# Optimization experiments

Measured on AMD Instinct MI355X. Metric: run time of the kernel, lower is better.

## Reference

```python
import jax, jax.numpy as jnp
import numpy as np

B, N_PATCH, DIM, HEADS = 64, 196, 768, 12
WIN = (14, 14)
NUM_REL_DIST = (2 * WIN[0] - 1) * (2 * WIN[1] - 1) + 3  # 732


def _build_rel_pos_index():
    ch, cw = np.arange(WIN[0]), np.arange(WIN[1])
    coords = np.stack(np.meshgrid(ch, cw, indexing='ij'))  # (2, Wh, Ww)
    flat = coords.reshape(2, -1)  # (2, Wh*Ww)
    rel = flat[:, :, None] - flat[:, None, :]  # (2, N, N)
    rel = rel.transpose(1, 2, 0).astype(np.int64)  # (N, N, 2)
    rel[:, :, 0] += WIN[0] - 1
    rel[:, :, 1] += WIN[1] - 1
    rel[:, :, 0] *= 2 * WIN[1] - 1
    n = WIN[0] * WIN[1] + 1
    idx = np.zeros((n, n), dtype=np.int64)
    idx[1:, 1:] = rel.sum(-1)
    idx[0, 0:] = NUM_REL_DIST - 3
    idx[0:, 0] = NUM_REL_DIST - 2
    idx[0, 0] = NUM_REL_DIST - 1
    return jnp.asarray(idx)


def setup_inputs() -> dict:
    key = jax.random.key(0)
    ks = jax.random.split(key, 6)
    d = DIM
    return {
        'x': jax.random.normal(ks[0], (B, N_PATCH + 1, d), dtype=jnp.float32),
        'qkv_w': jax.random.normal(ks[1], (3 * d, d), dtype=jnp.float32) * (d ** -0.5),
        'q_bias': jnp.zeros((d,), dtype=jnp.float32),
        'v_bias': jnp.zeros((d,), dtype=jnp.float32),
        'rpb_table': jax.random.normal(ks[2], (NUM_REL_DIST, HEADS), dtype=jnp.float32) * 0.02,
        'proj_w': jax.random.normal(ks[3], (d, d), dtype=jnp.float32) * (d ** -0.5),
        'proj_b': jnp.zeros((d,), dtype=jnp.float32),
        'rel_pos_index': _build_rel_pos_index(),
    }


def reference(x, qkv_w, q_bias, v_bias, rpb_table, proj_w, proj_b, rel_pos_index):
    Bn, N, C = x.shape
    H = HEADS
    hd = C // H
    scale = hd ** -0.5
    bias = jnp.concatenate([q_bias, jnp.zeros_like(v_bias), v_bias])
    qkv = x @ qkv_w.T + bias  # (B, N, 3C)
    qkv = qkv.reshape(Bn, N, 3, H, hd).transpose(2, 0, 3, 1, 4)  # (3, B, H, N, hd)
    q, k, v = qkv[0] * scale, qkv[1], qkv[2]
    attn = jnp.einsum('bhnd,bhmd->bhnm', q, k)  # (B, H, N, N)
    rpb = rpb_table[rel_pos_index.reshape(-1)].reshape(N, N, H).transpose(2, 0, 1)
    attn = jax.nn.softmax(attn + rpb[None], axis=-1)
    out = jnp.einsum('bhnm,bhmd->bhnd', attn, v)  # (B, H, N, hd)
    out = out.transpose(0, 2, 1, 3).reshape(Bn, N, C)
    return out @ proj_w.T + proj_b
```

## Files before the change

### kernel.cpp

```cpp
#include <hip/hip_runtime.h>
#include <hip/hip_bf16.h>

#define HEADS   12
#define HD      64
#define NTOK    197
#define BATCH   64
#define M_TOK   (BATCH*NTOK)
#define DIMC    768
#define NPAIR   (NTOK*NTOK)
#define MPAD    224

typedef __attribute__((ext_vector_type(8))) short bf16x8;
typedef __attribute__((ext_vector_type(4))) short s16x4;
typedef __attribute__((ext_vector_type(4))) float f32x4;

static __device__ __forceinline__ short f2bf(float f) {
    unsigned u = __float_as_uint(f);
    unsigned r = (u + 0x7FFFu + ((u >> 16) & 1u)) >> 16;
    return (short)r;
}
static __device__ __forceinline__ float bf2f(short s) {
    return __uint_as_float(((unsigned)(unsigned short)s) << 16);
}

#define NX (M_TOK * DIMC)
#define NW (3 * DIMC * DIMC)
#define NP (DIMC * DIMC)
__global__ void cvt_kernel(const float* __restrict__ s0, short* __restrict__ d0,
                           const float* __restrict__ s1, short* __restrict__ d1,
                           const float* __restrict__ s2, short* __restrict__ d2) {
    int i = (blockIdx.x * 256 + threadIdx.x) * 4;
    const float* s; short* d;
    if (i < NX)                { s = s0 + i; d = d0 + i; }
    else if (i < NX + NW)      { s = s1 + (i - NX); d = d1 + (i - NX); }
    else if (i < NX + NW + NP) { s = s2 + (i - NX - NW); d = d2 + (i - NX - NW); }
    else return;
    const float4 v = *(const float4*)s;
    s16x4 b; b[0] = f2bf(v.x); b[1] = f2bf(v.y); b[2] = f2bf(v.z); b[3] = f2bf(v.w);
    *(s16x4*)d = b;
}

#define NRPB (HEADS * 13 * 56 * 64)
__global__ void rpbl_kernel(const float* __restrict__ table,
                            const int* __restrict__ idx,
                            short* __restrict__ rpbl) {
    int i = blockIdx.x * 256 + threadIdx.x;
    if (i >= NRPB) return;
    const int lane = i & 63;
    const int q    = (i >> 6) % 56;
    const int rt   = ((i >> 6) / 56) % 13;
    const int h    = (i >> 6) / (56 * 13);
    const int rg = q / 14, mt = q - rg * 14;
    const int g = lane >> 4, c16 = lane & 15;
    const int n = rt * 16 + g * 4 + rg;
    const int m = mt * 16 + c16;
    float v = 0.f;
    if (n < NTOK && m < NTOK) v = table[idx[n * NTOK + m] * HEADS + h];
    rpbl[i] = f2bf(v);
}

#define STAGE(LA, LB, kt)                                                       \
    _Pragma("unroll")                                                           \
    for (int i = 0; i < 4; ++i) {                                               \
        __builtin_amdgcn_global_load_lds(                                       \
            (const __attribute__((address_space(1))) void*)(aptr[i] + (kt) * 64),\
            (__attribute__((address_space(3))) void*)&(LA)[(wv * 4 + i) * 512], \
            16, 0, 0);                                                          \
        __builtin_amdgcn_global_load_lds(                                       \
            (const __attribute__((address_space(1))) void*)(bptr[i] + (kt) * 64),\
            (__attribute__((address_space(3))) void*)&(LB)[(wv * 4 + i) * 512], \
            16, 0, 0);                                                          \
    }

#define COMPUTE(LA, LB)                                                         \
    _Pragma("unroll")                                                           \
    for (int ks = 0; ks < 2; ++ks) {                                            \
        bf16x8 af[4], bfr[4];                                                   \
        const int kk = (((ks * 4 + g) ^ (c16 & 7)) << 3);    \
        _Pragma("unroll")                                                       \
        for (int i = 0; i < 4; ++i)                                             \
            af[i] = *(const bf16x8*)&(LA)[(wr * 64 + i * 16 + c16) * 64 + kk];  \
        _Pragma("unroll")                                                       \
        for (int j = 0; j < 4; ++j)                                             \
            bfr[j] = *(const bf16x8*)&(LB)[(wc * 64 + j * 16 + c16) * 64 + kk]; \
        _Pragma("unroll")                                                       \
        for (int i = 0; i < 4; ++i)                                             \
            _Pragma("unroll")                                                   \
            for (int j = 0; j < 4; ++j)                                         \
                acc[i][j] = __builtin_amdgcn_mfma_f32_16x16x32_bf16(            \
                    af[i], bfr[j], acc[i][j], 0, 0, 0);                         \
    }

__global__ __launch_bounds__(256) void qkv_gemm_kernel(
    const short* __restrict__ xb, const short* __restrict__ wb,
    const float* __restrict__ qb, const float* __restrict__ vb,
    short* __restrict__ q_ws, short* __restrict__ k_ws,
    short* __restrict__ vt_ws) {
    __shared__ __align__(16) short lds_a0[128 * 64];
    __shared__ __align__(16) short lds_a1[128 * 64];
    __shared__ __align__(16) short lds_bb[2 * 128 * 64];
    const int tid  = threadIdx.x;
    const int lane = tid & 63;
    const int wv   = tid >> 6;
    const int wr   = wv >> 1, wc = wv & 1;
    const int flat = blockIdx.x;
    const int xcd  = flat & 7, pos = flat >> 3;
    const int swz  = ((xcd < 6) ? xcd * 223 : 1338 + (xcd - 6) * 222) + pos;
    const int bm   = swz / 18, bn = swz - bm * 18;
    const int g    = lane >> 4, c16 = lane & 15;

    f32x4 acc[4][4] = {};

    const int lrow = lane >> 3;
    const int lcol = ((lane & 7) ^ lrow) * 8;
    const short* aptr[4];
    const short* bptr[4];
    #pragma unroll
    for (int i = 0; i < 4; ++i) {
        const int r  = (wv * 4 + i) * 8 + lrow;
        int gr = bm * 128 + r; if (gr > M_TOK - 1) gr = M_TOK - 1;
        aptr[i] = xb + (size_t)gr * DIMC + lcol;
        bptr[i] = wb + (size_t)(bn * 128 + r) * DIMC + lcol;
    }

    STAGE(lds_a0, lds_bb, 0);
    __syncthreads();
    #pragma unroll
    for (int kp = 0; kp < 6; ++kp) {
        STAGE(lds_a1, (lds_bb + 8192), 2 * kp + 1);
        COMPUTE(lds_a0, lds_bb);
        __syncthreads();
        if (kp < 5) { STAGE(lds_a0, lds_bb, 2 * kp + 2); }
        COMPUTE(lds_a1, (lds_bb + 8192));
        if (kp < 5) __syncthreads();
    }

    __syncthreads();
    short* t = lds_bb;
    if (bn < 12) {
        const int isq = (bn < 6);
        #pragma unroll
        for (int j = 0; j < 4; ++j) {
            const int col = wc * 64 + j * 16 + c16;
            const int r   = isq ? bn * 128 + col : bn * 128 + col - DIMC;
            const float bias = isq ? qb[r] : 0.0f;
            #pragma unroll
            for (int i = 0; i < 4; ++i) {
                const int tok0 = wr * 64 + i * 16 + (g << 2);
                #pragma unroll
                for (int rg = 0; rg < 4; ++rg) {
                    const int tok = tok0 + rg;
                    const int sw  = ((tok >> 2) & 3) << 4;
                    float val = acc[i][j][rg];
                    if (isq) val = (val + bias) * 0.125f;
                    t[tok * 128 + (col ^ sw)] = f2bf(val);
                }
            }
        }
        __syncthreads();
        short* dst = isq ? q_ws : k_ws;
        const int rbase = isq ? bn * 128 : bn * 128 - DIMC;
        for (int tr = 0; tr < 32; ++tr) {
            const int tok = wv * 32 + tr;
            const int tt  = bm * 128 + tok;
            if (tt >= M_TOK) continue;
            const int bb = tt / NTOK, nn = tt - bb * NTOK;
            const int sw = ((tok >> 2) & 3) << 4;
            #pragma unroll
            for (int half = 0; half < 2; ++half) {
                const int col = half * 64 + lane;
                const int h   = (rbase + half * 64) >> 6;
                dst[(((size_t)bb * HEADS + h) * NTOK + nn) * HD + lane] =
                    t[tok * 128 + (col ^ sw)];
            }
        }
    } else {
        #pragma unroll
        for (int i = 0; i < 4; ++i) {
            const int lt0 = wr * 64 + i * 16 + (g << 2);
            #pragma unroll
            for (int j = 0; j < 4; ++j) {
                const int col  = wc * 64 + j * 16 + c16;
                const int sw   = (col & 7) << 3;
                const float bias = vb[(bn - 12) * 128 + col];
                #pragma unroll
                for (int rg = 0; rg < 4; ++rg)
                    t[col * 128 + ((lt0 + rg) ^ sw)] = f2bf(acc[i][j][rg] + bias);
            }
        }
        __syncthreads();
        for (int cc = 0; cc < 32; ++cc) {
            const int col = cc * 4 + wv;
            const int sw  = (col & 7) << 3;
            const int r   = bn * 128 + col - 1536;
            const int h   = r >> 6, d = r & 63;
            #pragma unroll
            for (int half = 0; half < 2; ++half) {
                const int lt = lane + half * 64;
                const int tt = bm * 128 + lt;
                if (tt < M_TOK) {
                    const int b = tt / NTOK, n = tt - b * NTOK;
                    vt_ws[(((size_t)b * HEADS + h) * HD + d) * MPAD + n] =
                        t[col * 128 + (lt ^ sw)];
                }
            }
        }
    }
}

__global__ __launch_bounds__(256) void attn_kernel(
    const short* __restrict__ q_ws, const short* __restrict__ k_ws,
    const short* __restrict__ vt_ws, const short* __restrict__ rpbL,
    short* __restrict__ o_ws) {
    __shared__ __align__(16) short p_lds[4 * 3712];
    const int lane = threadIdx.x & 63;
    const int wv   = threadIdx.x >> 6;
    const int id   = blockIdx.x;
    const int slot = id & 7;
    const int w    = (id >> 3) * 4 + wv;
    const int bhl  = w / 13;
    const int rt   = w - bhl * 13;
    const int bh   = bhl * 8 + slot;
    const int b    = bh / HEADS, h = bh - b * HEADS;
    const int g    = lane >> 4, c16 = lane & 15;
    short* p_base = p_lds + wv * 3712;

    bf16x8 qa0, qa1;
    {
        const size_t base = ((size_t)bh * NTOK + (rt * 16 + c16)) * HD + g * 8;
        qa0 = *(const bf16x8*)(q_ws + base);
        qa1 = *(const bf16x8*)(q_ws + base + 32);
    }

    bf16x8 kb0[14], kb1[14];
    #pragma unroll
    for (int mt = 0; mt < 14; ++mt) {
        const size_t base = ((size_t)bh * NTOK + (mt * 16 + c16)) * HD + g * 8;
        kb0[mt] = *(const bf16x8*)(k_ws + base);
        kb1[mt] = *(const bf16x8*)(k_ws + base + 32);
    }

    f32x4 sacc[14];
    #pragma unroll
    for (int t = 0; t < 14; ++t) sacc[t] = (f32x4){0.f, 0.f, 0.f, 0.f};
    #pragma unroll
    for (int mt = 0; mt < 14; ++mt) {
        sacc[mt] = __builtin_amdgcn_mfma_f32_16x16x32_bf16(qa0, kb0[mt], sacc[mt], 0, 0, 0);
        sacc[mt] = __builtin_amdgcn_mfma_f32_16x16x32_bf16(qa1, kb1[mt], sacc[mt], 0, 0, 0);
    }

    float rp[4][14];
    {
        const short* rb = rpbL + (((size_t)h * 13 + rt) * 56) * 64 + lane;
        #pragma unroll
        for (int rg = 0; rg < 4; ++rg)
            #pragma unroll
            for (int mt = 0; mt < 14; ++mt)
                rp[rg][mt] = bf2f(rb[(rg * 14 + mt) * 64]);
    }

    float mx[4] = {-1e30f, -1e30f, -1e30f, -1e30f};
    #pragma unroll
    for (int rg = 0; rg < 4; ++rg) {
        const int n = rt * 16 + g * 4 + rg;
        #pragma unroll
        for (int mt = 0; mt < 14; ++mt) {
            const int m = mt * 16 + c16;
            float s = (n < NTOK && m < NTOK) ? sacc[mt][rg] + rp[rg][mt] : -1e30f;
            sacc[mt][rg] = s;
            mx[rg] = fmaxf(mx[rg], s);
        }
    }
    #pragma unroll
    for (int off = 1; off < 16; off <<= 1)
        #pragma unroll
        for (int rg = 0; rg < 4; ++rg)
            mx[rg] = fmaxf(mx[rg], __shfl_xor(mx[rg], off, 64));

    float sm[4] = {0.f, 0.f, 0.f, 0.f};
    #pragma unroll
    for (int mt = 0; mt < 14; ++mt)
        #pragma unroll
        for (int rg = 0; rg < 4; ++rg) {
            float p = exp2f((sacc[mt][rg] - mx[rg]) * 1.44269504f);
            sm[rg] += p;
            p_base[(g * 4 + rg) * 232 + mt * 16 + c16] = f2bf(p);
        }

    bf16x8 vbf[7][4];
    #pragma unroll
    for (int ks = 0; ks < 7; ++ks)
        #pragma unroll
        for (int j = 0; j < 4; ++j)
            vbf[ks][j] = *(const bf16x8*)(vt_ws +
                ((size_t)bh * HD + j * 16 + c16) * MPAD + ks * 32 + g * 8);

    #pragma unroll
    for (int off = 1; off < 16; off <<= 1)
        #pragma unroll
        for (int rg = 0; rg < 4; ++rg)
            sm[rg] += __shfl_xor(sm[rg], off, 64);

    f32x4 oacc[4] = {};
    #pragma unroll
    for (int ks = 0; ks < 7; ++ks) {
        const int kk = ks * 32 + g * 8;
        bf16x8 pa = *(const bf16x8*)&p_base[c16 * 232 + kk];
        #pragma unroll
        for (int j = 0; j < 4; ++j)
            oacc[j] = __builtin_amdgcn_mfma_f32_16x16x32_bf16(pa, vbf[ks][j], oacc[j], 0, 0, 0);
    }

    #pragma unroll
    for (int rg = 0; rg < 4; ++rg) {
        const float inv = 1.0f / sm[rg];
        #pragma unroll
        for (int j = 0; j < 4; ++j)
            p_base[(g * 4 + rg) * 72 + j * 16 + c16] = f2bf(oacc[j][rg] * inv);
    }
    const size_t obase = ((size_t)b * NTOK) * DIMC + h * HD + lane;
    #pragma unroll
    for (int r = 0; r < 16; ++r) {
        const int n = rt * 16 + r;
        if (n < NTOK)
            o_ws[obase + (size_t)n * DIMC] = p_base[r * 72 + lane];
    }
}

__global__ __launch_bounds__(256) void proj_gemm_kernel(
    const short* __restrict__ a, const short* __restrict__ wb,
    const float* __restrict__ pb, float* __restrict__ out) {
    __shared__ __align__(16) short lds_a0[128 * 64];
    __shared__ __align__(16) short lds_a1[128 * 64];
    __shared__ __align__(16) short lds_b0[128 * 64];
    __shared__ __align__(16) short lds_b1[128 * 64];
    const int tid  = threadIdx.x;
    const int lane = tid & 63;
    const int wv   = tid >> 6;
    const int wr   = wv >> 1, wc = wv & 1;
    const int flat = blockIdx.x;
    const int xcd  = flat & 7, pos = flat >> 3;
    const int swz  = ((xcd < 2) ? xcd * 75 : 150 + (xcd - 2) * 74) + pos;
    const int bm   = swz / 6, bn = swz - bm * 6;
    const int g    = lane >> 4, c16 = lane & 15;

    f32x4 acc[4][4] = {};

    const int lrow = lane >> 3;
    const int lcol = ((lane & 7) ^ lrow) * 8;
    const short* aptr[4];
    const short* bptr[4];
    #pragma unroll
    for (int i = 0; i < 4; ++i) {
        const int r  = (wv * 4 + i) * 8 + lrow;
        int gr = bm * 128 + r; if (gr > M_TOK - 1) gr = M_TOK - 1;
        aptr[i] = a  + (size_t)gr * DIMC + lcol;
        bptr[i] = wb + (size_t)(bn * 128 + r) * DIMC + lcol;
    }

    STAGE(lds_a0, lds_b0, 0);
    __syncthreads();
    #pragma unroll
    for (int kp = 0; kp < 6; ++kp) {
        STAGE(lds_a1, lds_b1, 2 * kp + 1);
        COMPUTE(lds_a0, lds_b0);
        __syncthreads();
        if (kp < 5) { STAGE(lds_a0, lds_b0, 2 * kp + 2); }
        COMPUTE(lds_a1, lds_b1);
        if (kp < 5) __syncthreads();
    }

    #pragma unroll
    for (int i = 0; i < 4; ++i) {
        const int tbase = bm * 128 + wr * 64 + i * 16 + (g << 2);
        #pragma unroll
        for (int j = 0; j < 4; ++j) {
            const int c   = bn * 128 + wc * 64 + j * 16 + c16;
            const float bias = pb[c];
            #pragma unroll
            for (int rg = 0; rg < 4; ++rg) {
                const int tt = tbase + rg;
                if (tt >= M_TOK) continue;
                out[(size_t)tt * DIMC + c] = acc[i][j][rg] + bias;
            }
        }
    }
}

extern "C" void kernel_launch(void* const* d_in, const int* in_sizes, int n_in,
                              void* d_out, int out_size, void* d_ws, size_t ws_size,
                              hipStream_t stream) {
    const float* x       = (const float*)d_in[0];
    const float* qkv_w   = (const float*)d_in[1];
    const float* q_bias  = (const float*)d_in[2];
    const float* v_bias  = (const float*)d_in[3];
    const float* rpb_tab = (const float*)d_in[4];
    const float* proj_w  = (const float*)d_in[5];
    const float* proj_b  = (const float*)d_in[6];
    const int*   rel_idx = (const int*)d_in[7];
    float* out = (float*)d_out;

    char* ws = (char*)d_ws;
    short* q_ws     = (short*)(ws);
    short* k_ws     = (short*)(ws + 19368192);
    short* vt_ws    = (short*)(ws + 38736384);
    short* x_bf     = (short*)(ws + 60756480);
    short* o_ws     = (short*)(ws + 60756480);
    short* rpbL     = (short*)(ws + 80122368);
    short* w_bf     = (short*)(ws + 81985200);
    short* pw_bf    = (short*)(ws + 85524144);

    const int ncvt = (NX + NW + NP) / 4;
    cvt_kernel<<<(ncvt + 255) / 256, 256, 0, stream>>>(x, x_bf, qkv_w, w_bf, proj_w, pw_bf);
    rpbl_kernel<<<(NRPB + 255) / 256, 256, 0, stream>>>(rpb_tab, rel_idx, rpbL);

    qkv_gemm_kernel<<<1782, 256, 0, stream>>>(x_bf, w_bf, q_bias, v_bias,
                                              q_ws, k_ws, vt_ws);
    attn_kernel<<<2496, 256, 0, stream>>>(q_ws, k_ws, vt_ws, rpbL, o_ws);
    proj_gemm_kernel<<<594, 256, 0, stream>>>(o_ws, pw_bf, proj_b, out);
}
```

Measured before the change: 183.6 us.

## Use triple-buffered K=32 pipeline with vmcnt waits in QKV and proj GEMMs

```diff
diff --git a/kernel.cpp b/kernel.cpp
--- a/kernel.cpp
+++ b/kernel.cpp
@@ -59,30 +59,29 @@
     rpbl[i] = f2bf(v);
 }
 
-#define STAGE(LA, LB, kt)                                                       \
+#define STAGE32(B, kt)                                                          \
     _Pragma("unroll")                                                           \
-    for (int i = 0; i < 4; ++i) {                                               \
+    for (int i = 0; i < 2; ++i) {                                               \
         __builtin_amdgcn_global_load_lds(                                       \
-            (const __attribute__((address_space(1))) void*)(aptr[i] + (kt) * 64),\
-            (__attribute__((address_space(3))) void*)&(LA)[(wv * 4 + i) * 512], \
+            (const __attribute__((address_space(1))) void*)(aptr[i] + (kt) * 32),\
+            (__attribute__((address_space(3))) void*)&lds[(B) * 8192 + (wv * 2 + i) * 512], \
             16, 0, 0);                                                          \
         __builtin_amdgcn_global_load_lds(                                       \
-            (const __attribute__((address_space(1))) void*)(bptr[i] + (kt) * 64),\
-            (__attribute__((address_space(3))) void*)&(LB)[(wv * 4 + i) * 512], \
+            (const __attribute__((address_space(1))) void*)(bptr[i] + (kt) * 32),\
+            (__attribute__((address_space(3))) void*)&lds[(B) * 8192 + 4096 + (wv * 2 + i) * 512], \
             16, 0, 0);                                                          \
     }
 
-#define COMPUTE(LA, LB)                                                         \
-    _Pragma("unroll")                                                           \
-    for (int ks = 0; ks < 2; ++ks) {                                            \
+#define COMPUTE32(B)                                                            \
+    {                                                                           \
         bf16x8 af[4], bfr[4];                                                   \
-        const int kk = (((ks * 4 + g) ^ (c16 & 7)) << 3);    \
+        const int cs = ((g - (c16 >> 1)) & 3) << 3;     \
         _Pragma("unroll")                                                       \
         for (int i = 0; i < 4; ++i)                                             \
-            af[i] = *(const bf16x8*)&(LA)[(wr * 64 + i * 16 + c16) * 64 + kk];  \
+            af[i] = *(const bf16x8*)&lds[(B) * 8192 + (wr * 64 + i * 16 + c16) * 32 + cs]; \
         _Pragma("unroll")                                                       \
         for (int j = 0; j < 4; ++j)                                             \
-            bfr[j] = *(const bf16x8*)&(LB)[(wc * 64 + j * 16 + c16) * 64 + kk]; \
+            bfr[j] = *(const bf16x8*)&lds[(B) * 8192 + 4096 + (wc * 64 + j * 16 + c16) * 32 + cs]; \
         _Pragma("unroll")                                                       \
         for (int i = 0; i < 4; ++i)                                             \
             _Pragma("unroll")                                                   \
@@ -91,14 +90,24 @@
                     af[i], bfr[j], acc[i][j], 0, 0, 0);                         \
     }
 
+#define GEMM_LOOP32()                                                           \
+    STAGE32(0, 0);                                                              \
+    STAGE32(1, 1);                                                              \
+    _Pragma("unroll")                                                           \
+    for (int t = 0; t < 24; ++t) {                                              \
+        if (t == 23) { asm volatile("s_waitcnt vmcnt(0)" ::: "memory"); }       \
+        else         { asm volatile("s_waitcnt vmcnt(4)" ::: "memory"); }       \
+        __builtin_amdgcn_s_barrier();                                           \
+        COMPUTE32(t % 3);                                                       \
+        if (t + 2 < 24) { STAGE32((t + 2) % 3, t + 2); }                        \
+    }
+
 __global__ __launch_bounds__(256) void qkv_gemm_kernel(
     const short* __restrict__ xb, const short* __restrict__ wb,
     const float* __restrict__ qb, const float* __restrict__ vb,
     short* __restrict__ q_ws, short* __restrict__ k_ws,
     short* __restrict__ vt_ws) {
-    __shared__ __align__(16) short lds_a0[128 * 64];
-    __shared__ __align__(16) short lds_a1[128 * 64];
-    __shared__ __align__(16) short lds_bb[2 * 128 * 64];
+    __shared__ __align__(16) short lds[3 * 8192];
     const int tid  = threadIdx.x;
     const int lane = tid & 63;
     const int wv   = tid >> 6;
@@ -111,32 +120,22 @@
 
     f32x4 acc[4][4] = {};
 
-    const int lrow = lane >> 3;
-    const int lcol = ((lane & 7) ^ lrow) * 8;
-    const short* aptr[4];
-    const short* bptr[4];
-    #pragma unroll
-    for (int i = 0; i < 4; ++i) {
-        const int r  = (wv * 4 + i) * 8 + lrow;
+    const int lrow32 = lane >> 2;
+    const int lchunk = ((lane & 3) + (lane >> 3)) & 3;
+    const short* aptr[2];
+    const short* bptr[2];
+    #pragma unroll
+    for (int i = 0; i < 2; ++i) {
+        const int r  = (wv * 2 + i) * 16 + lrow32;
         int gr = bm * 128 + r; if (gr > M_TOK - 1) gr = M_TOK - 1;
-        aptr[i] = xb + (size_t)gr * DIMC + lcol;
-        bptr[i] = wb + (size_t)(bn * 128 + r) * DIMC + lcol;
-    }
-
-    STAGE(lds_a0, lds_bb, 0);
+        aptr[i] = xb + (size_t)gr * DIMC + lchunk * 8;
+        bptr[i] = wb + (size_t)(bn * 128 + r) * DIMC + lchunk * 8;
+    }
+
+    GEMM_LOOP32();
+
     __syncthreads();
-    #pragma unroll
-    for (int kp = 0; kp < 6; ++kp) {
-        STAGE(lds_a1, (lds_bb + 8192), 2 * kp + 1);
-        COMPUTE(lds_a0, lds_bb);
-        __syncthreads();
-        if (kp < 5) { STAGE(lds_a0, lds_bb, 2 * kp + 2); }
-        COMPUTE(lds_a1, (lds_bb + 8192));
-        if (kp < 5) __syncthreads();
-    }
-
-    __syncthreads();
-    short* t = lds_bb;
+    short* t = lds;
     if (bn < 12) {
         const int isq = (bn < 6);
         #pragma unroll
@@ -330,10 +329,7 @@
 __global__ __launch_bounds__(256) void proj_gemm_kernel(
     const short* __restrict__ a, const short* __restrict__ wb,
     const float* __restrict__ pb, float* __restrict__ out) {
-    __shared__ __align__(16) short lds_a0[128 * 64];
-    __shared__ __align__(16) short lds_a1[128 * 64];
-    __shared__ __align__(16) short lds_b0[128 * 64];
-    __shared__ __align__(16) short lds_b1[128 * 64];
+    __shared__ __align__(16) short lds[3 * 8192];
     const int tid  = threadIdx.x;
     const int lane = tid & 63;
     const int wv   = tid >> 6;
@@ -346,29 +342,19 @@
 
     f32x4 acc[4][4] = {};
 
-    const int lrow = lane >> 3;
-    const int lcol = ((lane & 7) ^ lrow) * 8;
-    const short* aptr[4];
-    const short* bptr[4];
-    #pragma unroll
-    for (int i = 0; i < 4; ++i) {
-        const int r  = (wv * 4 + i) * 8 + lrow;
+    const int lrow32 = lane >> 2;
+    const int lchunk = ((lane & 3) + (lane >> 3)) & 3;
+    const short* aptr[2];
+    const short* bptr[2];
+    #pragma unroll
+    for (int i = 0; i < 2; ++i) {
+        const int r  = (wv * 2 + i) * 16 + lrow32;
         int gr = bm * 128 + r; if (gr > M_TOK - 1) gr = M_TOK - 1;
-        aptr[i] = a  + (size_t)gr * DIMC + lcol;
-        bptr[i] = wb + (size_t)(bn * 128 + r) * DIMC + lcol;
-    }
-
-    STAGE(lds_a0, lds_b0, 0);
-    __syncthreads();
-    #pragma unroll
-    for (int kp = 0; kp < 6; ++kp) {
-        STAGE(lds_a1, lds_b1, 2 * kp + 1);
-        COMPUTE(lds_a0, lds_b0);
-        __syncthreads();
-        if (kp < 5) { STAGE(lds_a0, lds_b0, 2 * kp + 2); }
-        COMPUTE(lds_a1, lds_b1);
-        if (kp < 5) __syncthreads();
-    }
+        aptr[i] = a  + (size_t)gr * DIMC + lchunk * 8;
+        bptr[i] = wb + (size_t)(bn * 128 + r) * DIMC + lchunk * 8;
+    }
+
+    GEMM_LOOP32();
 
     #pragma unroll
     for (int i = 0; i < 4; ++i) {
```

Result: no change. 183.2 us (-0.2%).
